# Kernel tuning notes

Measured on AMD Instinct MI355X. Metric: run time of the kernel, lower is better.

Reference implementation:

```python
import jax, jax.numpy as jnp
import numpy as np

NUM_HEADS = 16
NEG_INF = jnp.float32(-1e9)


def setup_inputs() -> dict:
    key = jax.random.key(0)
    ks = jax.random.split(key, 4)
    B, N, C = 2, 2048, 1024
    s_in = 1.0 / np.sqrt(C)
    return {
        "x": jax.random.normal(ks[0], (B, N, C), jnp.float32),
        "attention_mask": jnp.ones((B, N, N), jnp.int32),
        "qkv_w": jax.random.normal(ks[1], (3 * C, C), jnp.float32) * s_in,
        "qkv_b": jnp.zeros((3 * C,), jnp.float32),
        "proj_w": jax.random.normal(ks[2], (C, C), jnp.float32) * s_in,
        "proj_b": jnp.zeros((C,), jnp.float32),
    }


def reference(x, attention_mask, qkv_w, qkv_b, proj_w, proj_b):
    B, N, C = x.shape
    H = NUM_HEADS
    D = C // H
    scale = D ** -0.5
    # fused QKV projection (torch Linear: x @ W^T + b)
    qkv = (x @ qkv_w.T + qkv_b).reshape(B, N, 3, H, D)
    qkv = jnp.transpose(qkv, (2, 0, 3, 1, 4))  # [3, B, H, N, D]
    q, k, v = qkv[0], qkv[1], qkv[2]
    # scaled dot-product scores [B, H, N, N]
    attn = jnp.einsum("bhnd,bhmd->bhnm", q, k) * scale
    # padding mask: [B, N, N] broadcast over heads
    attn = jnp.where(attention_mask[:, None, :, :] == 0, NEG_INF, attn)
    # causal mask
    causal = jnp.triu(jnp.ones((N, N), bool), k=1)
    attn = jnp.where(causal, NEG_INF, attn)
    w = jax.nn.softmax(attn, axis=-1)
    out = jnp.einsum("bhnm,bhmd->bhnd", w, v)
    out = jnp.transpose(out, (0, 2, 1, 3)).reshape(B, N, C)
    return out @ proj_w.T + proj_b
```

## Files before the change

### kernel.cpp

```cpp
#include <hip/hip_runtime.h>
#include <hip/hip_bf16.h>


typedef __bf16 bf16x8 __attribute__((ext_vector_type(8)));
typedef __bf16 bf16x4 __attribute__((ext_vector_type(4)));
typedef __bf16 bf16x2 __attribute__((ext_vector_type(2)));
typedef float  f32x4  __attribute__((ext_vector_type(4)));
typedef float  f32x16 __attribute__((ext_vector_type(16)));
typedef int    i32x4  __attribute__((ext_vector_type(4)));

#define MFMA16(a, b, c) __builtin_amdgcn_mfma_f32_16x16x32_bf16((a), (b), (c), 0, 0, 0)

__device__ __forceinline__ void async_copy16(const __bf16* g, __bf16* l) {
    __builtin_amdgcn_global_load_lds(
        (const __attribute__((address_space(1))) void*)g,
        (__attribute__((address_space(3))) void*)l,
        16, 0, 0);
}

__device__ __forceinline__ unsigned packbf(float a, float b) {
    union { bf16x2 v; unsigned u; } un;
    un.v[0] = (__bf16)a; un.v[1] = (__bf16)b;
    return un.u;
}

__global__ void f32_to_bf16_3k(const float* __restrict__ a, __bf16* __restrict__ ad, int na,
                               const float* __restrict__ b, __bf16* __restrict__ bd, int nb,
                               const float* __restrict__ c, __bf16* __restrict__ cd, int nc)
{
    int i = blockIdx.x * blockDim.x + threadIdx.x;
    const float* src; __bf16* dst; int j;
    if (i < na)            { src = a; dst = ad; j = i; }
    else if (i < na + nb)  { src = b; dst = bd; j = i - na; }
    else if (i < na + nb + nc) { src = c; dst = cd; j = i - na - nb; }
    else return;
    float4 v = reinterpret_cast<const float4*>(src)[j];
    bf16x4 o;
    o[0] = (__bf16)v.x; o[1] = (__bf16)v.y; o[2] = (__bf16)v.z; o[3] = (__bf16)v.w;
    reinterpret_cast<bf16x4*>(dst)[j] = o;
}

__global__ void mask_reduce_k(const int* __restrict__ mask, int* __restrict__ mflag) {
    __shared__ int ok;
    const int t = threadIdx.x;
    if (t == 0) ok = 1;
    __syncthreads();
    const int jt = blockIdx.x & 31;
    const int it = (blockIdx.x >> 5) & 31;
    const int b  = blockIdx.x >> 10;
    bool all1 = true;
#pragma unroll
    for (int c = 0; c < 4; ++c) {
        const int row = c * 16 + (t >> 4);
        const int col = (t & 15) * 4;
        const int4 v = *reinterpret_cast<const int4*>(
            &mask[((size_t)(b * 2048 + it * 64 + row)) * 2048 + jt * 64 + col]);
        all1 = all1 && v.x && v.y && v.z && v.w;
    }
    if (!all1) ok = 0;
    __syncthreads();
    if (t == 0) mflag[(b * 32 + it) * 32 + jt] = ok;
}

#define BAR() asm volatile("s_barrier" ::: "memory")
#define VM2() asm volatile("s_waitcnt vmcnt(2)" ::: "memory")

__global__ __launch_bounds__(512, 2) void gemm_qkv8_k(
    const __bf16* __restrict__ A, const __bf16* __restrict__ Bm,
    const float* __restrict__ bias,
    __bf16* __restrict__ qg, __bf16* __restrict__ kg, __bf16* __restrict__ vtg)
{
    __shared__ __align__(16) __bf16 As[2][16384];
    __shared__ __align__(16) __bf16 Bs[2][16384];

    const int t = threadIdx.x;
    const int lane = t & 63;
    const int w = t >> 6;
    const int wr = w >> 2, wc = w & 3;
    const int li = lane & 15, g = lane >> 4;

    const int bid = (blockIdx.x & 7) * 24 + (blockIdx.x >> 3);
    const int m0 = (bid / 12) << 8;
    const int n0 = (bid % 12) << 8;

    const int srow = t >> 3;
    const int scol = ((t & 7) ^ (srow & 7)) << 3;
    const __bf16* pA = A  + (size_t)(m0 + srow) * 1024 + scol;
    const __bf16* pB = Bm + (size_t)(n0 + srow) * 1024 + scol;
    __bf16* dA = &As[0][0] + t * 8;
    __bf16* dB = &Bs[0][0] + t * 8;

#define STAGE_A(BB, T, HH) do {                                                   \
    const size_t ro_ = (size_t)((HH) * 128) * 1024 + (size_t)(T) * 64;            \
    async_copy16(pA + ro_,         dA + (BB) * 16384 + (HH) * 8192);              \
    async_copy16(pA + ro_ + 65536, dA + (BB) * 16384 + (HH) * 8192 + 4096);       \
  } while (0)
#define STAGE_B(BB, T, HH) do {                                                   \
    const size_t ro_ = (size_t)((HH) * 128) * 1024 + (size_t)(T) * 64;            \
    async_copy16(pB + ro_,         dB + (BB) * 16384 + (HH) * 8192);              \
    async_copy16(pB + ro_ + 65536, dB + (BB) * 16384 + (HH) * 8192 + 4096);       \
  } while (0)

    const int aoff0 = ((0 + g) ^ (li & 7)) << 3;
    const int aoff1 = ((4 + g) ^ (li & 7)) << 3;
    const int abase = (wr * 128 + li) * 64;
    const int bbase = (wc * 64 + li) * 64;

    f32x4 acc[8][4] = {};
    bf16x8 a[4][2], b[2][2][2];

#define READ_A(BB, MH) do { _Pragma("unroll")                                     \
    for (int mi2 = 0; mi2 < 4; ++mi2) {                                           \
      const __bf16* p_ = &As[BB][abase + ((MH) * 4 + mi2) * 1024];                \
      a[mi2][0] = *reinterpret_cast<const bf16x8*>(p_ + aoff0);                   \
      a[mi2][1] = *reinterpret_cast<const bf16x8*>(p_ + aoff1); } } while (0)
#define READ_B(BB, NH) do { _Pragma("unroll")                                     \
    for (int ni2 = 0; ni2 < 2; ++ni2) {                                           \
      const __bf16* p_ = &Bs[BB][bbase + ((NH) * 2 + ni2) * 1024];                \
      b[NH][ni2][0] = *reinterpret_cast<const bf16x8*>(p_ + aoff0);               \
      b[NH][ni2][1] = *reinterpret_cast<const bf16x8*>(p_ + aoff1); } } while (0)
#define MFMA_QUAD(MH, NH) do {                                                    \
    __builtin_amdgcn_s_setprio(1);                                                \
    _Pragma("unroll") for (int mi2 = 0; mi2 < 4; ++mi2)                           \
    _Pragma("unroll") for (int ni2 = 0; ni2 < 2; ++ni2) {                         \
      f32x4 c_ = acc[(MH) * 4 + mi2][(NH) * 2 + ni2];                             \
      c_ = MFMA16(a[mi2][0], b[NH][ni2][0], c_);                                  \
      c_ = MFMA16(a[mi2][1], b[NH][ni2][1], c_);                                  \
      acc[(MH) * 4 + mi2][(NH) * 2 + ni2] = c_; }                                 \
    __builtin_amdgcn_s_setprio(0); } while (0)

#define KTILE(BB, T) do {                                                         \
    const int Tn_  = ((T) + 1 < 16) ? (T) + 1 : 15;                               \
    const int Tn2_ = ((T) + 2 < 16) ? (T) + 2 : 15;                               \
    STAGE_A((BB) ^ 1, Tn_, 1);                                                    \
    READ_A(BB, 0); READ_B(BB, 0);                                                 \
    BAR(); MFMA_QUAD(0, 0); BAR();                                                \
    STAGE_B((BB) ^ 1, Tn_, 0);                                                    \
    READ_B(BB, 1);                                                                \
    BAR(); MFMA_QUAD(0, 1); BAR();                                                \
    STAGE_B((BB) ^ 1, Tn_, 1);                                                    \
    READ_A(BB, 1);                                                                \
    BAR(); MFMA_QUAD(1, 0); BAR();                                                \
    STAGE_A((BB), Tn2_, 0);                                                       \
    VM2(); BAR(); MFMA_QUAD(1, 1); BAR();                                         \
  } while (0)

    STAGE_A(0, 0, 0); STAGE_A(0, 0, 1);
    STAGE_B(0, 0, 0); STAGE_B(0, 0, 1);
    STAGE_A(1, 1, 0);
    VM2(); BAR();

#pragma unroll 1
    for (int jj = 0; jj < 8; ++jj) {
        KTILE(0, 2 * jj);
        KTILE(1, 2 * jj + 1);
    }

    const int nbase = n0 + wc * 64;
    const int s = nbase >> 10;
    const int headg = (m0 >> 11) * 16 + ((nbase & 1023) >> 6);
    const int mrow = (m0 & 2047) + wr * 128 + g * 4;
    float bv[4];
#pragma unroll
    for (int ni = 0; ni < 4; ++ni) bv[ni] = bias[nbase + ni * 16 + li];

    if (s == 2) {
#pragma unroll
        for (int mi = 0; mi < 8; ++mi) {
#pragma unroll
            for (int ni = 0; ni < 4; ++ni) {
                bf16x4 st;
#pragma unroll
                for (int r = 0; r < 4; ++r) st[r] = (__bf16)(acc[mi][ni][r] + bv[ni]);
                *reinterpret_cast<bf16x4*>(
                    &vtg[((size_t)(headg * 64) + ni * 16 + li) * 2048 + mrow + mi * 16]) = st;
            }
        }
    } else {
        __bf16* og = (s == 0) ? qg : kg;
        const float sc = (s == 0) ? 0.18033688f : 1.0f;
#pragma unroll
        for (int mi = 0; mi < 8; ++mi) {
#pragma unroll
            for (int r = 0; r < 4; ++r) {
                __bf16* rp = og + ((size_t)headg * 2048 + mrow + mi * 16 + r) * 64;
#pragma unroll
                for (int ni = 0; ni < 4; ++ni)
                    rp[ni * 16 + li] = (__bf16)((acc[mi][ni][r] + bv[ni]) * sc);
            }
        }
    }
#undef KTILE
#undef MFMA_QUAD
#undef READ_A
#undef READ_B
#undef STAGE_A
#undef STAGE_B
}

__global__ __launch_bounds__(256) void gemm_proj_k(
    const __bf16* __restrict__ A, const __bf16* __restrict__ Bm,
    const float* __restrict__ bias, int M, int N, int K,
    float* __restrict__ outf)
{
    __shared__ __align__(16) __bf16 As[128 * 64];
    __shared__ __align__(16) __bf16 Bs[128 * 64];
    const int t = threadIdx.x;
    const int nb = N >> 7;
    const int m0 = (blockIdx.x / nb) << 7;
    const int n0 = (blockIdx.x % nb) << 7;
    const int lane = t & 63, w = t >> 6;
    const int g = lane >> 4, li = lane & 15;
    const int wr = w >> 1, wc = w & 1;
    const __bf16* Ab = A + (size_t)m0 * K;
    const __bf16* Bb = Bm + (size_t)n0 * K;

    f32x4 acc[4][4] = {};

    for (int k0 = 0; k0 < K; k0 += 64) {
#pragma unroll
        for (int c = 0; c < 4; ++c) {
            const int e = (c * 256 + t) * 8;
            const int row = e >> 6;
            const int col = e & 63;
            async_copy16(Ab + (size_t)row * K + k0 + col, As + e);
            async_copy16(Bb + (size_t)row * K + k0 + col, Bs + e);
        }
        __syncthreads();
#pragma unroll
        for (int kk = 0; kk < 2; ++kk) {
            bf16x8 af[4], bf[4];
#pragma unroll
            for (int mi = 0; mi < 4; ++mi)
                af[mi] = *reinterpret_cast<const bf16x8*>(
                    &As[(wr * 64 + mi * 16 + li) * 64 + kk * 32 + g * 8]);
#pragma unroll
            for (int ni = 0; ni < 4; ++ni)
                bf[ni] = *reinterpret_cast<const bf16x8*>(
                    &Bs[(wc * 64 + ni * 16 + li) * 64 + kk * 32 + g * 8]);
#pragma unroll
            for (int mi = 0; mi < 4; ++mi)
#pragma unroll
                for (int ni = 0; ni < 4; ++ni)
                    acc[mi][ni] = MFMA16(af[mi], bf[ni], acc[mi][ni]);
        }
        __syncthreads();
    }

#pragma unroll
    for (int mi = 0; mi < 4; ++mi) {
#pragma unroll
        for (int ni = 0; ni < 4; ++ni) {
            const int n = n0 + wc * 64 + ni * 16 + li;
            const float bv = bias[n];
#pragma unroll
            for (int r = 0; r < 4; ++r) {
                const int m = m0 + wr * 64 + mi * 16 + g * 4 + r;
                outf[(size_t)m * N + n] = acc[mi][ni][r] + bv;
            }
        }
    }
}

__global__ __launch_bounds__(512) void attn_k(
    const __bf16* __restrict__ qg, const __bf16* __restrict__ kg,
    const __bf16* __restrict__ vtg, const int* __restrict__ mflag,
    const int* __restrict__ mask, __bf16* __restrict__ ao)
{
    __shared__ __align__(16) __bf16 Ks[4][4096];
    __shared__ __align__(16) __bf16 Vs[4][4096];
    __shared__ __align__(16) __bf16 Ps[8][1024];
    const int t = threadIdx.x;
    const int w = t >> 6, lane = t & 63;
    const int li = lane & 15, g = lane >> 4;
    const int xcd = blockIdx.x & 7;
    const int idx = blockIdx.x >> 3;
    const int hg  = xcd * 4 + (idx & 3);
    const int band = 15 - (idx >> 2);
    const int bI = hg >> 4, hI = hg & 15;
    const int iq = band * 128 + w * 16 + li;
    const int mydiag = 2 * band + (w >> 2);
    const int ktmax = 2 * band + 1;
    const int rowt = 2 * band + (w >> 2);
    const size_t hoff = (size_t)hg * (2048 * 64);
    const __bf16* qh = qg + hoff;
    const __bf16* kh = kg + hoff;
    const __bf16* vh = vtg + hoff;
    char* pw = (char*)&Ps[w][0];
    const int sw7 = li & 7;

    bf16x8 qf[2];
#pragma unroll
    for (int half = 0; half < 2; ++half)
        qf[half] = *reinterpret_cast<const bf16x8*>(&qh[(size_t)iq * 64 + half * 32 + g * 8]);

    f32x4 o[4] = {};
    float mrun = -1e30f, lrun = 0.0f;

#define STAGE(BUF, KT) do {                                                       \
    const int p_ = t * 16;                                                        \
    const int row_ = p_ >> 7, sl_ = (p_ >> 4) & 7;                                \
    const int gc_ = (sl_ ^ (row_ & 7)) << 3;                                      \
    async_copy16(kh + (size_t)(((KT) << 6) + row_) * 64 + gc_,                    \
                 (__bf16*)((char*)(&Ks[0][0]) + (BUF) * 8192 + p_));              \
    async_copy16(vh + (size_t)row_ * 2048 + ((KT) << 6) + gc_,                    \
                 (__bf16*)((char*)(&Vs[0][0]) + (BUF) * 8192 + p_));              \
} while (0)

    STAGE(0, 0);
    STAGE(1, 1);
    VM2();
    __builtin_amdgcn_s_barrier();

    int cur = 0;
    for (int kt = 0; kt <= ktmax; ++kt) {
        if (kt + 2 <= ktmax) {
            STAGE((cur + 2) & 3, kt + 2);
            VM2();
        } else {
            asm volatile("s_waitcnt vmcnt(0)" ::: "memory");
        }
        __builtin_amdgcn_sched_barrier(0);
        __builtin_amdgcn_s_barrier();
        __builtin_amdgcn_sched_barrier(0);
        if (kt <= mydiag) {
            const char* kb = (char*)&Ks[0][0] + cur * 8192;
            const char* vb = (char*)&Vs[0][0] + cur * 8192;
            f32x4 s[4] = {};
            __builtin_amdgcn_s_setprio(1);
#pragma unroll
            for (int kb_ = 0; kb_ < 4; ++kb_) {
                const int row = kb_ * 16 + li;
#pragma unroll
                for (int half = 0; half < 2; ++half) {
                    bf16x8 kf = *reinterpret_cast<const bf16x8*>(
                        kb + row * 128 + (((half * 4 + g) ^ sw7) << 4));
                    s[kb_] = MFMA16(kf, qf[half], s[kb_]);
                }
            }
            __builtin_amdgcn_s_setprio(0);
            const bool pflag = (mflag[(bI * 32 + rowt) * 32 + kt] == 0);
            if (pflag || kt == mydiag) {
                const int jb = kt * 64;
#pragma unroll
                for (int kb_ = 0; kb_ < 4; ++kb_)
#pragma unroll
                    for (int r = 0; r < 4; ++r) {
                        const int j0 = jb + kb_ * 16 + 4 * g + r;
                        float v0 = s[kb_][r];
                        if (j0 > iq ||
                            (pflag && mask[((size_t)(bI * 2048 + iq)) * 2048 + j0] == 0))
                            v0 = -1e30f;
                        s[kb_][r] = v0;
                    }
            }
            float mt = fmaxf(fmaxf(s[0][0], s[0][1]), fmaxf(s[0][2], s[0][3]));
#pragma unroll
            for (int kb_ = 1; kb_ < 4; ++kb_)
                mt = fmaxf(mt, fmaxf(fmaxf(s[kb_][0], s[kb_][1]),
                                     fmaxf(s[kb_][2], s[kb_][3])));
            mt = fmaxf(mt, __shfl_xor(mt, 16));
            mt = fmaxf(mt, __shfl_xor(mt, 32));
            if (!__all(mt <= mrun + 8.0f)) {
                const float mn = fmaxf(mrun, mt);
                const float alpha = exp2f(mrun - mn);
#pragma unroll
                for (int df = 0; df < 4; ++df)
#pragma unroll
                    for (int r = 0; r < 4; ++r) o[df][r] *= alpha;
                lrun *= alpha;
                mrun = mn;
            }
#pragma unroll
            for (int kb_ = 0; kb_ < 4; ++kb_)
#pragma unroll
                for (int r = 0; r < 4; ++r) {
                    const float p = exp2f(s[kb_][r] - mrun);
                    s[kb_][r] = p;
                    lrun += p;
                }
#pragma unroll
            for (int kb_ = 0; kb_ < 4; ++kb_) {
                const unsigned lo = packbf(s[kb_][0], s[kb_][1]);
                const unsigned hi = packbf(s[kb_][2], s[kb_][3]);
                *reinterpret_cast<uint2*>(
                    pw + li * 128 + (((2 * kb_ + (g >> 1)) ^ sw7) << 4) + ((g & 1) << 3)) =
                    make_uint2(lo, hi);
            }
            bf16x8 pb[2];
#pragma unroll
            for (int ks = 0; ks < 2; ++ks)
                pb[ks] = *reinterpret_cast<const bf16x8*>(
                    pw + li * 128 + (((4 * ks + g) ^ sw7) << 4));
            __builtin_amdgcn_s_setprio(1);
#pragma unroll
            for (int df = 0; df < 4; ++df) {
                const int vrow = df * 16 + li;
#pragma unroll
                for (int ks = 0; ks < 2; ++ks) {
                    bf16x8 vf = *reinterpret_cast<const bf16x8*>(
                        vb + vrow * 128 + (((4 * ks + g) ^ sw7) << 4));
                    o[df] = MFMA16(vf, pb[ks], o[df]);
                }
            }
            __builtin_amdgcn_s_setprio(0);
        }
        cur = (cur + 1) & 3;
    }
#undef STAGE

    lrun += __shfl_xor(lrun, 16);
    lrun += __shfl_xor(lrun, 32);
    const float inv = 1.0f / lrun;
    __bf16* aor = ao + ((size_t)(bI * 2048 + iq)) * 1024 + hI * 64 + g * 4;
#pragma unroll
    for (int df = 0; df < 4; ++df) {
        bf16x4 st;
#pragma unroll
        for (int r = 0; r < 4; ++r) st[r] = (__bf16)(o[df][r] * inv);
        *reinterpret_cast<bf16x4*>(&aor[df * 16]) = st;
    }
}

extern "C" void kernel_launch(void* const* d_in, const int* in_sizes, int n_in,
                              void* d_out, int out_size, void* d_ws, size_t ws_size,
                              hipStream_t stream)
{
    const float* x      = (const float*)d_in[0];
    const int*   mask   = (const int*)d_in[1];
    const float* qkv_w  = (const float*)d_in[2];
    const float* qkv_b  = (const float*)d_in[3];
    const float* proj_w = (const float*)d_in[4];
    const float* proj_b = (const float*)d_in[5];
    float* out = (float*)d_out;

    char* ws = (char*)d_ws;
    __bf16* xb    = (__bf16*)(ws + 0);
    __bf16* wqkv  = (__bf16*)(ws + 8388608);
    __bf16* wproj = (__bf16*)(ws + 14680064);
    __bf16* qg    = (__bf16*)(ws + 16777216);
    __bf16* kg    = (__bf16*)(ws + 25165824);
    __bf16* vtg   = (__bf16*)(ws + 33554432);
    __bf16* ao    = (__bf16*)(ws + 41943040);
    int*    mflag = (int*)(ws + 50331648);

    f32_to_bf16_3k<<<8192, 256, 0, stream>>>(x, xb, 1048576,
                                             qkv_w, wqkv, 786432,
                                             proj_w, wproj, 262144);
    mask_reduce_k<<<2 * 32 * 32, 256, 0, stream>>>(mask, mflag);
    gemm_qkv8_k<<<192, 512, 0, stream>>>(xb, wqkv, qkv_b, qg, kg, vtg);
    attn_k<<<512, 512, 0, stream>>>(qg, kg, vtg, mflag, mask, ao);
    gemm_proj_k<<<32 * 8, 256, 0, stream>>>(ao, wproj, proj_b, 4096, 1024, 1024, out);
}
```

Measured before the change: 134.3 us.

## Pipeline projection GEMM with triple-buffered swizzled LDS and reorder attention bands

The projection GEMM is rewritten with 128x64 tiles, giving 512 blocks instead of 256 to fill the CUs better. It stages loads into a three-deep LDS ring using async loads, an XOR swizzle to avoid bank conflicts, partial vmcnt waits and a single barrier per k-step, and it raises MFMA priority with setprio. Block IDs are remapped across XCDs. Separately, the attention kernel now interleaves heavy and light causal bands (descending then ascending) to balance load across the grid. The risks are more blocks re-reading the A matrix and possible race windows from the single barrier per step with three buffers.

```diff
diff --git a/kernel.cpp b/kernel.cpp
--- a/kernel.cpp
+++ b/kernel.cpp
@@ -64,6 +64,7 @@
 
 #define BAR() asm volatile("s_barrier" ::: "memory")
 #define VM2() asm volatile("s_waitcnt vmcnt(2)" ::: "memory")
+#define VM6() asm volatile("s_waitcnt vmcnt(6)" ::: "memory")
 
 __global__ __launch_bounds__(512, 2) void gemm_qkv8_k(
     const __bf16* __restrict__ A, const __bf16* __restrict__ Bm,
@@ -200,63 +201,94 @@
 
 __global__ __launch_bounds__(256) void gemm_proj_k(
     const __bf16* __restrict__ A, const __bf16* __restrict__ Bm,
-    const float* __restrict__ bias, int M, int N, int K,
-    float* __restrict__ outf)
+    const float* __restrict__ bias, float* __restrict__ outf)
 {
-    __shared__ __align__(16) __bf16 As[128 * 64];
-    __shared__ __align__(16) __bf16 Bs[128 * 64];
+    __shared__ __align__(16) __bf16 As[3][8192];
+    __shared__ __align__(16) __bf16 Bs[3][4096];
     const int t = threadIdx.x;
-    const int nb = N >> 7;
-    const int m0 = (blockIdx.x / nb) << 7;
-    const int n0 = (blockIdx.x % nb) << 7;
     const int lane = t & 63, w = t >> 6;
-    const int g = lane >> 4, li = lane & 15;
+    const int li = lane & 15, g = lane >> 4;
     const int wr = w >> 1, wc = w & 1;
-    const __bf16* Ab = A + (size_t)m0 * K;
-    const __bf16* Bb = Bm + (size_t)n0 * K;
-
-    f32x4 acc[4][4] = {};
-
-    for (int k0 = 0; k0 < K; k0 += 64) {
-#pragma unroll
-        for (int c = 0; c < 4; ++c) {
-            const int e = (c * 256 + t) * 8;
-            const int row = e >> 6;
-            const int col = e & 63;
-            async_copy16(Ab + (size_t)row * K + k0 + col, As + e);
-            async_copy16(Bb + (size_t)row * K + k0 + col, Bs + e);
-        }
-        __syncthreads();
-#pragma unroll
-        for (int kk = 0; kk < 2; ++kk) {
-            bf16x8 af[4], bf[4];
-#pragma unroll
-            for (int mi = 0; mi < 4; ++mi)
-                af[mi] = *reinterpret_cast<const bf16x8*>(
-                    &As[(wr * 64 + mi * 16 + li) * 64 + kk * 32 + g * 8]);
-#pragma unroll
-            for (int ni = 0; ni < 4; ++ni)
-                bf[ni] = *reinterpret_cast<const bf16x8*>(
-                    &Bs[(wc * 64 + ni * 16 + li) * 64 + kk * 32 + g * 8]);
-#pragma unroll
-            for (int mi = 0; mi < 4; ++mi)
-#pragma unroll
-                for (int ni = 0; ni < 4; ++ni)
-                    acc[mi][ni] = MFMA16(af[mi], bf[ni], acc[mi][ni]);
-        }
-        __syncthreads();
-    }
+    const int sw7 = li & 7;
+    const int bid = (blockIdx.x & 7) * 64 + (blockIdx.x >> 3);
+    const int m0 = (bid >> 4) << 7;
+    const int n0 = (bid & 15) << 6;
+
+#define PSTAGE(BUF, KT) do {                                                      \
+    _Pragma("unroll")                                                             \
+    for (int c_ = 0; c_ < 4; ++c_) {                                              \
+        const int row_ = c_ * 32 + (t >> 3);                                      \
+        async_copy16(A + (size_t)(m0 + row_) * 1024 + ((KT) << 6)                 \
+                       + (((t & 7) ^ (row_ & 7)) << 3),                           \
+                     &As[BUF][0] + c_ * 2048 + t * 8);                            \
+    }                                                                             \
+    _Pragma("unroll")                                                             \
+    for (int c_ = 0; c_ < 2; ++c_) {                                              \
+        const int row_ = c_ * 32 + (t >> 3);                                      \
+        async_copy16(Bm + (size_t)(n0 + row_) * 1024 + ((KT) << 6)                \
+                       + (((t & 7) ^ (row_ & 7)) << 3),                           \
+                     &Bs[BUF][0] + c_ * 2048 + t * 8);                            \
+    }                                                                             \
+} while (0)
+
+    f32x4 acc[4][2] = {};
+
+    PSTAGE(0, 0);
+    int cur = 0;
+    for (int kt = 0; kt < 16; ++kt) {
+        int nxt = cur + 1; if (nxt == 3) nxt = 0;
+        if (kt < 15) {
+            PSTAGE(nxt, kt + 1);
+            VM6();
+        } else {
+            asm volatile("s_waitcnt vmcnt(0)" ::: "memory");
+        }
+        __builtin_amdgcn_sched_barrier(0);
+        __builtin_amdgcn_s_barrier();
+        __builtin_amdgcn_sched_barrier(0);
+
+        bf16x8 af[4][2], bf[2][2];
+#pragma unroll
+        for (int mi = 0; mi < 4; ++mi) {
+            const int ra = wr * 64 + mi * 16 + li;
+#pragma unroll
+            for (int kk = 0; kk < 2; ++kk)
+                af[mi][kk] = *reinterpret_cast<const bf16x8*>(
+                    (char*)&As[cur][0] + ra * 128 + (((kk * 4 + g) ^ sw7) << 4));
+        }
+#pragma unroll
+        for (int ni = 0; ni < 2; ++ni) {
+            const int rb = wc * 32 + ni * 16 + li;
+#pragma unroll
+            for (int kk = 0; kk < 2; ++kk)
+                bf[ni][kk] = *reinterpret_cast<const bf16x8*>(
+                    (char*)&Bs[cur][0] + rb * 128 + (((kk * 4 + g) ^ sw7) << 4));
+        }
+        __builtin_amdgcn_s_setprio(1);
+#pragma unroll
+        for (int mi = 0; mi < 4; ++mi)
+#pragma unroll
+            for (int ni = 0; ni < 2; ++ni) {
+                f32x4 c_ = acc[mi][ni];
+                c_ = MFMA16(af[mi][0], bf[ni][0], c_);
+                c_ = MFMA16(af[mi][1], bf[ni][1], c_);
+                acc[mi][ni] = c_;
+            }
+        __builtin_amdgcn_s_setprio(0);
+        cur = nxt;
+    }
+#undef PSTAGE
 
 #pragma unroll
     for (int mi = 0; mi < 4; ++mi) {
 #pragma unroll
-        for (int ni = 0; ni < 4; ++ni) {
-            const int n = n0 + wc * 64 + ni * 16 + li;
+        for (int ni = 0; ni < 2; ++ni) {
+            const int n = n0 + wc * 32 + ni * 16 + li;
             const float bv = bias[n];
 #pragma unroll
             for (int r = 0; r < 4; ++r) {
                 const int m = m0 + wr * 64 + mi * 16 + g * 4 + r;
-                outf[(size_t)m * N + n] = acc[mi][ni][r] + bv;
+                outf[(size_t)m * 1024 + n] = acc[mi][ni][r] + bv;
             }
         }
     }
@@ -276,7 +308,8 @@
     const int xcd = blockIdx.x & 7;
     const int idx = blockIdx.x >> 3;
     const int hg  = xcd * 4 + (idx & 3);
-    const int band = 15 - (idx >> 2);
+    const int q_  = idx >> 2;
+    const int band = (q_ < 8) ? (15 - q_) : (q_ - 8);
     const int bI = hg >> 4, hI = hg & 15;
     const int iq = band * 128 + w * 16 + li;
     const int mydiag = 2 * band + (w >> 2);
@@ -450,5 +483,5 @@
     mask_reduce_k<<<2 * 32 * 32, 256, 0, stream>>>(mask, mflag);
     gemm_qkv8_k<<<192, 512, 0, stream>>>(xb, wqkv, qkv_b, qg, kg, vtg);
     attn_k<<<512, 512, 0, stream>>>(qg, kg, vtg, mflag, mask, ao);
-    gemm_proj_k<<<32 * 8, 256, 0, stream>>>(ao, wproj, proj_b, 4096, 1024, 1024, out);
-}
+    gemm_proj_k<<<512, 256, 0, stream>>>(ao, wproj, proj_b, out);
+}
```

Result: faster. 121.4 us (-9.6%).
